# Optimization experiments

Measured on AMD Instinct MI355X. Metric: run time of the kernel, lower is better.

## Reference

```python
import jax, jax.numpy as jnp
import numpy as np

B, S, D = 2, 2048, 768          # batch, n_ctx, d_model
NQK, DQK = 12, 64               # n_qk_heads, d_qk_head
NOV, DOV = 768, 1               # n_ov_heads, d_ov_head
R = NOV // NQK                  # OV heads per QK head
VKV = 4                         # virtual_kv_num
BASE = 10000.0
SCALE = DQK ** 0.5              # cfg.attn_scale default


def _rotary_sin_cos():
    # TransformerLens-style (non-adjacent-pairs): freq repeated as (2 d)
    pos = jnp.arange(S, dtype=jnp.float32)
    freq = BASE ** (jnp.arange(0, DQK, 2, dtype=jnp.float32) / DQK)
    freq = jnp.concatenate([freq, freq])          # [DQK]
    angles = pos[:, None] / freq[None, :]         # [S, DQK]
    return jnp.sin(angles), jnp.cos(angles)


def _apply_rotary(x, sin, cos):
    # x: [b, pos, head, DQK]; rotary_dim == d_qk_head so full rotation
    half = DQK // 2
    rot = jnp.concatenate([-x[..., half:], x[..., :half]], axis=-1)
    return x * cos[None, :, None, :] + rot * sin[None, :, None, :]


def setup_inputs() -> dict:
    key = jax.random.key(0)
    ks = jax.random.split(key, 7)
    std_qk = (2.0 / (D * DQK)) ** 0.5   # kaiming fan_in (d_model*d_head)
    std_ov = (2.0 / (D * DOV)) ** 0.5
    std_o = (2.0 / (DOV * D)) ** 0.5
    sin, cos = _rotary_sin_cos()
    return {
        "resid": jax.random.normal(ks[0], (B, S, D), jnp.float32),
        "W_Q": jax.random.normal(ks[1], (NQK, D, DQK), jnp.float32) * std_qk,
        "W_K": jax.random.normal(ks[2], (NQK, D, DQK), jnp.float32) * std_qk,
        "W_V": jax.random.normal(ks[3], (NOV, D, DOV), jnp.float32) * std_ov,
        "W_O": jax.random.normal(ks[4], (NOV, DOV, D), jnp.float32) * std_o,
        "b_Q": jnp.zeros((NQK, DQK), jnp.float32),
        "b_K": jnp.zeros((NQK, DQK), jnp.float32),
        "b_V": jnp.zeros((NOV, DOV), jnp.float32),
        "virtual_k": jax.random.normal(ks[5], (VKV, NQK, DQK), jnp.float32) * (2.0 / (NQK * DQK)) ** 0.5,
        "virtual_v": jnp.zeros((VKV, NOV, DOV), jnp.float32),  # init zeros, requires_grad=False
        "rotary_sin": sin,
        "rotary_cos": cos,
    }


def reference(resid, W_Q, W_K, W_V, W_O, b_Q, b_K, b_V,
              virtual_k, virtual_v, rotary_sin, rotary_cos):
    # q/k/v projections: per-head low-rank maps + bias  -> [b, s, h, d]
    q = jnp.einsum('bsm,hmd->bshd', resid, W_Q) + b_Q
    k = jnp.einsum('bsm,hmd->bshd', resid, W_K) + b_K
    v = jnp.einsum('bsm,hmd->bshd', resid, W_V) + b_V
    # rotary on q and k
    q = _apply_rotary(q, rotary_sin, rotary_cos)
    k = _apply_rotary(k, rotary_sin, rotary_cos)
    # append virtual KV tokens at the end of the key axis
    k = jnp.concatenate([k, jnp.broadcast_to(virtual_k[None], (B, VKV, NQK, DQK))], axis=1)
    v = jnp.concatenate([v, jnp.broadcast_to(virtual_v[None], (B, VKV, NOV, DOV))], axis=1)
    # full attention scores [b, nqk, S, S+VKV]
    scores = jnp.einsum('bqhd,bkhd->bhqk', q, k) / SCALE
    # causal mask: tril(ones(S, S+VKV), diagonal=VKV) -> key j visible iff j <= i + VKV
    qi = jnp.arange(S)[:, None]
    kj = jnp.arange(S + VKV)[None, :]
    mask = kj <= qi + VKV
    scores = jnp.where(mask[None, None], scores, -jnp.inf)
    pattern = jax.nn.softmax(scores, axis=-1)
    pattern = jnp.where(jnp.isnan(pattern), 0.0, pattern)
    # group OV heads by QK head: v [b, k, NOV, DOV] -> [b, NQK, R, k, DOV]
    v_r = jnp.transpose(v, (0, 2, 1, 3)).reshape(B, NQK, R, S + VKV, DOV)
    z = jnp.einsum('bnqk,bnrkh->bnrqh', pattern, v_r)       # [b, NQK, R, S, DOV]
    z = z.reshape(B, NOV, S, DOV).transpose(0, 2, 1, 3)      # [b, S, NOV, DOV]
    out = jnp.einsum('bqhd,hdm->bqm', z, W_O)                # cal_out (no b_O)
    return out
```

## Files before the change

### kernel.cpp

```cpp
#include <hip/hip_runtime.h>

typedef __attribute__((ext_vector_type(8))) __bf16 bf16x8;
typedef __attribute__((ext_vector_type(4))) __bf16 bf16x4;
typedef __attribute__((ext_vector_type(4))) float  f32x4;

__device__ __forceinline__ void gld_lds16(const void* g, void* l) {
  __builtin_amdgcn_global_load_lds(
      (const __attribute__((address_space(1))) unsigned int*)g,
      (__attribute__((address_space(3))) unsigned int*)l, 16, 0, 0);
}

template<int N>
__device__ __forceinline__ void wait_vmcnt() {
  if constexpr (N == 0)      asm volatile("s_waitcnt vmcnt(0)" ::: "memory");
  else if constexpr (N == 4) asm volatile("s_waitcnt vmcnt(4)" ::: "memory");
  else if constexpr (N == 6) asm volatile("s_waitcnt vmcnt(6)" ::: "memory");
  else if constexpr (N == 8) asm volatile("s_waitcnt vmcnt(8)" ::: "memory");
}

#define QSCALE 0.18033688011112042f

__global__ __launch_bounds__(256) void prep_kernel(
    const float* __restrict__ resid, const float* __restrict__ WV,
    __bf16* __restrict__ Rb, __bf16* __restrict__ Wt1)
{
  int t = blockIdx.x * 256 + threadIdx.x;
  if (t < 786432) {
    f32x4 v = *(const f32x4*)(resid + (size_t)t * 4);
    bf16x4 o;
#pragma unroll
    for (int j = 0; j < 4; ++j) o[j] = (__bf16)v[j];
    *(bf16x4*)(Rb + (size_t)t * 4) = o;
    return;
  }
  t -= 786432;
  if (t < 73728) {
    const float* vp = WV + (size_t)t * 8;
    f32x4 v0 = *(const f32x4*)vp, v1 = *(const f32x4*)(vp + 4);
    bf16x8 o;
#pragma unroll
    for (int j = 0; j < 8; ++j) o[j] = (__bf16)((j < 4) ? v0[j & 3] : v1[j & 3]);
    *(bf16x8*)(Wt1 + (size_t)1536 * 768 + (size_t)t * 8) = o;
  }
}

__global__ __launch_bounds__(256) void wtrans_kernel(
    const float* __restrict__ WQ, const float* __restrict__ WK,
    const float* __restrict__ WO,
    __bf16* __restrict__ Wt1, __bf16* __restrict__ Wt2)
{
  __shared__ float tile[64][65];
  int g = blockIdx.x, tid = threadIdx.x;
  const float* src; __bf16* dst;
  int sld, dld, r0, c0, drow0, dcol0;
  if (g < 288) {
    const float* W = (g < 144) ? WQ : WK;
    int gg = g % 144;
    int h = gg / 12, kt = gg - h * 12;
    src = W + (size_t)h * 49152; sld = 64; r0 = kt * 64; c0 = 0;
    dst = Wt1; dld = 768;
    drow0 = ((g < 144) ? 0 : 768) + h * 64; dcol0 = kt * 64;
  } else {
    int gg = g - 288;
    int rt = gg / 12, ct = gg - rt * 12;
    src = WO; sld = 768; r0 = rt * 64; c0 = ct * 64;
    dst = Wt2; dld = 768; drow0 = ct * 64; dcol0 = rt * 64;
  }
#pragma unroll
  for (int c = 0; c < 4; ++c) {
    int li = c * 256 + tid;
    int r = li >> 4, cc = (li & 15) * 4;
    f32x4 v = *(const f32x4*)(src + (size_t)(r0 + r) * sld + c0 + cc);
#pragma unroll
    for (int j = 0; j < 4; ++j) tile[r][cc + j] = v[j];
  }
  __syncthreads();
#pragma unroll
  for (int c = 0; c < 2; ++c) {
    int li = c * 256 + tid;
    int cc = li >> 3, rr = (li & 7) * 8;
    bf16x8 o;
#pragma unroll
    for (int j = 0; j < 8; ++j) o[j] = (__bf16)tile[rr + j][cc];
    *(bf16x8*)(dst + (size_t)(drow0 + cc) * dld + dcol0 + rr) = o;
  }
}

template<int OUTF, int BN>
__global__ __launch_bounds__(256) void gemm_bt(
    const __bf16* __restrict__ A, const __bf16* __restrict__ Bt,
    void* __restrict__ C, int M, int N, int K, int ldc)
{
  constexpr int LDSB = BN * 128;
  constexpr int BUF  = 16384 + LDSB;
  constexpr int BSTG = BN / 32;
  constexpr int NLD  = 4 + BSTG;
  constexpr int IM   = (BN == 128) ? 4 : 2;
  __shared__ __align__(16) char smem[2 * BUF];
  const int tid = threadIdx.x;
  const int l = tid & 63, wv = tid >> 6;
  const int l15 = l & 15, lg = l >> 4;
  const int wmb = (BN == 128) ? (wv >> 1) * 64 : wv * 32;
  const int wnb = (BN == 128) ? (wv & 1) * 64 : 0;
  const int m0 = blockIdx.y * 128, n0 = blockIdx.x * BN;
  const int sw = (l15 & 7) << 4;

  auto stage = [&](int buf, int k0) {
    char* a_l = smem + buf * BUF;
    char* b_l = a_l + 16384;
#pragma unroll
    for (int c = 0; c < 4; ++c) {
      int i2 = c * 256 + tid;
      int row = i2 >> 3, slt = i2 & 7;
      gld_lds16(A + (size_t)(m0 + row) * K + k0 + ((slt ^ (row & 7)) * 8), a_l + i2 * 16);
    }
#pragma unroll
    for (int c = 0; c < BSTG; ++c) {
      int i2 = c * 256 + tid;
      int row = i2 >> 3, slt = i2 & 7;
      gld_lds16(Bt + (size_t)(n0 + row) * K + k0 + ((slt ^ (row & 7)) * 8), b_l + i2 * 16);
    }
  };

  f32x4 acc[IM][4] = {};
  stage(0, 0);
  int cur = 0;
  for (int k0 = 0; k0 < K; k0 += 64) {
    const bool has_next = (k0 + 64 < K);
    if (has_next) stage(cur ^ 1, k0 + 64);
    if (has_next) wait_vmcnt<NLD>(); else wait_vmcnt<0>();
    __builtin_amdgcn_s_barrier();
    __builtin_amdgcn_sched_barrier(0);
    char* a_lds = smem + cur * BUF;
    char* b_lds = a_lds + 16384;
#pragma unroll
    for (int kk = 0; kk < 2; ++kk) {
      bf16x8 af[IM], bfr[4];
#pragma unroll
      for (int i = 0; i < IM; ++i) {
        int mr = wmb + i * 16 + l15;
        af[i] = *(const bf16x8*)(a_lds + mr * 128 + ((lg * 16 + kk * 64) ^ sw));
      }
#pragma unroll
      for (int j = 0; j < 4; ++j) {
        int nr = wnb + j * 16 + l15;
        bfr[j] = *(const bf16x8*)(b_lds + nr * 128 + ((lg * 16 + kk * 64) ^ sw));
      }
#pragma unroll
      for (int i = 0; i < IM; ++i)
#pragma unroll
        for (int j = 0; j < 4; ++j)
          acc[i][j] = __builtin_amdgcn_mfma_f32_16x16x32_bf16(af[i], bfr[j], acc[i][j], 0, 0, 0);
    }
    __builtin_amdgcn_s_barrier();
    cur ^= 1;
  }
#pragma unroll
  for (int i = 0; i < IM; ++i)
#pragma unroll
    for (int j = 0; j < 4; ++j)
#pragma unroll
      for (int r = 0; r < 4; ++r) {
        int row = m0 + wmb + i * 16 + lg * 4 + r;
        int col = n0 + wnb + j * 16 + l15;
        if (OUTF) ((float*)C)[(size_t)row * ldc + col] = acc[i][j][r];
        else      ((__bf16*)C)[(size_t)row * ldc + col] = (__bf16)acc[i][j][r];
      }
}

__global__ __launch_bounds__(256) void qk_rotary(
    const __bf16* __restrict__ qkv, const float* __restrict__ bQ,
    const float* __restrict__ bK, const float* __restrict__ vk,
    const float* __restrict__ rsin, const float* __restrict__ rcos,
    __bf16* __restrict__ Qb, __bf16* __restrict__ Kb)
{
  int t = blockIdx.x * 256 + threadIdx.x;
  if (t < 196608) {
    int d0 = (t & 3) * 8;
    int x = t >> 2;
    int bh = x >> 11, s = x & 2047;
    int b = bh / 12, h = bh - b * 12;
    const __bf16* rowp = qkv + ((size_t)(b * 2048 + s)) * 2304 + h * 64;
    bf16x8 ql = *(const bf16x8*)(rowp + d0);
    bf16x8 qu = *(const bf16x8*)(rowp + d0 + 32);
    bf16x8 kl = *(const bf16x8*)(rowp + 768 + d0);
    bf16x8 ku = *(const bf16x8*)(rowp + 768 + d0 + 32);
    const float* bql = bQ + h * 64 + d0;
    const float* bkl = bK + h * 64 + d0;
    const float* snp = rsin + s * 64 + d0;
    const float* csp = rcos + s * 64 + d0;
    f32x4 bq0 = *(const f32x4*)(bql),      bq1 = *(const f32x4*)(bql + 4);
    f32x4 bq2 = *(const f32x4*)(bql + 32), bq3 = *(const f32x4*)(bql + 36);
    f32x4 bk0 = *(const f32x4*)(bkl),      bk1 = *(const f32x4*)(bkl + 4);
    f32x4 bk2 = *(const f32x4*)(bkl + 32), bk3 = *(const f32x4*)(bkl + 36);
    f32x4 sl0 = *(const f32x4*)(snp),      sl1 = *(const f32x4*)(snp + 4);
    f32x4 su0 = *(const f32x4*)(snp + 32), su1 = *(const f32x4*)(snp + 36);
    f32x4 cl0 = *(const f32x4*)(csp),      cl1 = *(const f32x4*)(csp + 4);
    f32x4 cu0 = *(const f32x4*)(csp + 32), cu1 = *(const f32x4*)(csp + 36);
    bf16x8 qlo, quo, klo, kuo;
#pragma unroll
    for (int j = 0; j < 8; ++j) {
      float snl = (j < 4) ? sl0[j & 3] : sl1[j & 3];
      float csl = (j < 4) ? cl0[j & 3] : cl1[j & 3];
      float snu = (j < 4) ? su0[j & 3] : su1[j & 3];
      float csu = (j < 4) ? cu0[j & 3] : cu1[j & 3];
      float q1 = (float)ql[j] + ((j < 4) ? bq0[j & 3] : bq1[j & 3]);
      float q2 = (float)qu[j] + ((j < 4) ? bq2[j & 3] : bq3[j & 3]);
      float k1 = (float)kl[j] + ((j < 4) ? bk0[j & 3] : bk1[j & 3]);
      float k2 = (float)ku[j] + ((j < 4) ? bk2[j & 3] : bk3[j & 3]);
      qlo[j] = (__bf16)((q1 * csl - q2 * snl) * QSCALE);
      quo[j] = (__bf16)((q2 * csu + q1 * snu) * QSCALE);
      klo[j] = (__bf16)(k1 * csl - k2 * snl);
      kuo[j] = (__bf16)(k2 * csu + k1 * snu);
    }
    __bf16* qb = Qb + ((size_t)bh * 2048 + s) * 64;
    __bf16* kb = Kb + ((size_t)bh * 2112 + s) * 64;
    *(bf16x8*)(qb + d0) = qlo;  *(bf16x8*)(qb + d0 + 32) = quo;
    *(bf16x8*)(kb + d0) = klo;  *(bf16x8*)(kb + d0 + 32) = kuo;
    return;
  }
  t -= 196608;
  if (t < 12288) {
    int d0 = (t & 7) * 8;
    int x = t >> 3;
    int bh = x >> 6, sp = x & 63;
    int h = bh % 12;
    bf16x8 o;
    if (sp < 4) {
      const float* vp = vk + ((size_t)sp * 12 + h) * 64 + d0;
      f32x4 v0 = *(const f32x4*)(vp), v1 = *(const f32x4*)(vp + 4);
#pragma unroll
      for (int j = 0; j < 8; ++j) o[j] = (__bf16)((j < 4) ? v0[j & 3] : v1[j & 3]);
    } else {
#pragma unroll
      for (int j = 0; j < 8; ++j) o[j] = (__bf16)0.0f;
    }
    *(bf16x8*)(Kb + ((size_t)bh * 2112 + 2048 + sp) * 64 + d0) = o;
  }
}

__global__ __launch_bounds__(256) void v_trans(
    const __bf16* __restrict__ qkv, const float* __restrict__ bV,
    const float* __restrict__ vv, __bf16* __restrict__ Vt)
{
  __shared__ float tile[64][65];
  int st = blockIdx.x, bh = blockIdx.y;
  int b = bh / 12, h = bh - b * 12;
  int tid = threadIdx.x;
#pragma unroll
  for (int c = 0; c < 2; ++c) {
    int chunk = c * 256 + tid;
    int srow = chunk >> 3, d0 = (chunk & 7) * 8;
    int s = st * 64 + srow;
    float vals[8];
    if (s < 2048) {
      bf16x8 v8 = *(const bf16x8*)(qkv + ((size_t)(b * 2048 + s)) * 2304 + 1536 + h * 64 + d0);
      const float* bvp = bV + h * 64 + d0;
      f32x4 b0 = *(const f32x4*)(bvp), b1 = *(const f32x4*)(bvp + 4);
#pragma unroll
      for (int j = 0; j < 8; ++j) vals[j] = (float)v8[j] + ((j < 4) ? b0[j & 3] : b1[j & 3]);
    } else if (s < 2052) {
      const float* vp = vv + (size_t)(s - 2048) * 768 + h * 64 + d0;
      f32x4 v0 = *(const f32x4*)(vp), v1 = *(const f32x4*)(vp + 4);
#pragma unroll
      for (int j = 0; j < 8; ++j) vals[j] = (j < 4) ? v0[j & 3] : v1[j & 3];
    } else {
#pragma unroll
      for (int j = 0; j < 8; ++j) vals[j] = 0.0f;
    }
#pragma unroll
    for (int j = 0; j < 8; ++j) tile[srow][d0 + j] = vals[j];
  }
  __syncthreads();
#pragma unroll
  for (int c = 0; c < 2; ++c) {
    int chunk = c * 256 + tid;
    int drow = chunk >> 3, s0 = (chunk & 7) * 8;
    bf16x8 o8;
#pragma unroll
    for (int j = 0; j < 8; ++j) o8[j] = (__bf16)tile[s0 + j][drow];
    *(bf16x8*)(Vt + ((size_t)bh * 64 + drow) * 2112 + st * 64 + s0) = o8;
  }
}

__global__ __launch_bounds__(256) void attn_kernel(
    const __bf16* __restrict__ Qb, const __bf16* __restrict__ Kb,
    const __bf16* __restrict__ Vt, __bf16* __restrict__ Opart,
    float* __restrict__ Lsum)
{
  __shared__ __align__(16) char smem[40960];
  char* p_lds = smem + 32768;
  const int tid = threadIdx.x;
  const int l = tid & 63, w = tid >> 6;
  const int l15 = l & 15, lg = l >> 4;
  const int idx = blockIdx.x;
  const int bh = idx % 24;
  int pidx = idx / 24;
  int qt = 31, rem = pidx;
  for (;;) { int c = (qt + 9) >> 3; if (rem < c) break; rem -= c; --qt; }
  const int ts = rem * 8;
  const int te = min(ts + 8, qt + 2);
  const int slot = bh * 84 + pidx;
  const int q16 = qt * 64 + w * 16;
  const int sw = (l15 & 7) << 4;
  const int qrow = w * 16 + l15;

  const __bf16* Kbase = Kb + (size_t)bh * 2112 * 64;
  const __bf16* Vbase = Vt + (size_t)bh * 64 * 2112;

  auto stage = [&](int buf, int kt0) {
    char* k_l = smem + buf * 16384;
    char* v_l = k_l + 8192;
#pragma unroll
    for (int c = 0; c < 2; ++c) {
      int i2 = c * 256 + tid;
      int row = i2 >> 3, slt = i2 & 7;
      gld_lds16(Kbase + (kt0 + row) * 64 + ((slt ^ (row & 7)) * 8), k_l + i2 * 16);
    }
#pragma unroll
    for (int c = 0; c < 2; ++c) {
      int i2 = c * 256 + tid;
      int row = i2 >> 3, slt = i2 & 7;
      gld_lds16(Vbase + row * 2112 + kt0 + ((slt ^ (row & 7)) * 8), v_l + i2 * 16);
    }
  };

  stage(0, ts * 64);

  const __bf16* qp = Qb + ((size_t)bh * 2048 + q16 + l15) * 64 + lg * 8;
  const bf16x8 qa0 = *(const bf16x8*)qp;
  const bf16x8 qa1 = *(const bf16x8*)(qp + 32);

  f32x4 o[4] = {};
  float lrun = 0.0f;

  int cur = 0;
  for (int kt = ts; kt < te; ++kt) {
    const int kt0 = kt * 64;
    const bool has_next = (kt + 1 < te);
    if (has_next) stage(cur ^ 1, kt0 + 64);
    if (has_next) wait_vmcnt<4>(); else wait_vmcnt<0>();
    __builtin_amdgcn_s_barrier();
    __builtin_amdgcn_sched_barrier(0);
    char* k_lds = smem + cur * 16384;
    char* v_lds = k_lds + 8192;

    if (kt0 <= q16 + 19) {
      f32x4 sfr[4];
#pragma unroll
      for (int kb = 0; kb < 4; ++kb) {
        int krow = kb * 16 + l15;
        f32x4 a = {};
        bf16x8 ka0 = *(const bf16x8*)(k_lds + krow * 128 + ((lg * 16) ^ sw));
        bf16x8 ka1 = *(const bf16x8*)(k_lds + krow * 128 + ((lg * 16 + 64) ^ sw));
        a = __builtin_amdgcn_mfma_f32_16x16x32_bf16(ka0, qa0, a, 0, 0, 0);
        a = __builtin_amdgcn_mfma_f32_16x16x32_bf16(ka1, qa1, a, 0, 0, 0);
        sfr[kb] = a;
      }
      if (kt >= qt) {
        int qlim = q16 + l15 + 4;
#pragma unroll
        for (int kb = 0; kb < 4; ++kb)
#pragma unroll
          for (int r = 0; r < 4; ++r) {
            int kg = kt0 + kb * 16 + lg * 4 + r;
            if (kg > qlim || kg >= 2052) sfr[kb][r] = -1e30f;
          }
      }
      float rsum = 0.0f;
#pragma unroll
      for (int kb = 0; kb < 4; ++kb) {
        bf16x4 pv;
#pragma unroll
        for (int r = 0; r < 4; ++r) {
          float p = exp2f(sfr[kb][r]);
          rsum += p;
          pv[r] = (__bf16)p;
        }
        *(bf16x4*)(p_lds + qrow * 128 + ((kb * 32 + lg * 8) ^ sw)) = pv;
      }
      rsum += __shfl_xor(rsum, 16);
      rsum += __shfl_xor(rsum, 32);
      lrun += rsum;
#pragma unroll
      for (int kblk = 0; kblk < 2; ++kblk) {
        bf16x8 pa = *(const bf16x8*)(p_lds + qrow * 128 + ((kblk * 64 + lg * 16) ^ sw));
#pragma unroll
        for (int dv = 0; dv < 4; ++dv) {
          int vrow = dv * 16 + l15;
          bf16x8 vb = *(const bf16x8*)(v_lds + vrow * 128 + ((kblk * 64 + lg * 16) ^ sw));
          o[dv] = __builtin_amdgcn_mfma_f32_16x16x32_bf16(pa, vb, o[dv], 0, 0, 0);
        }
      }
    }
    __builtin_amdgcn_s_barrier();
    cur ^= 1;
  }
  if (lg == 0) Lsum[slot * 64 + qrow] = lrun;
  __bf16* op = Opart + (size_t)slot * 4096;
#pragma unroll
  for (int dv = 0; dv < 4; ++dv)
#pragma unroll
    for (int r = 0; r < 4; ++r)
      op[(w * 16 + lg * 4 + r) * 64 + dv * 16 + l15] = (__bf16)o[dv][r];
}

__global__ __launch_bounds__(256) void attn_merge(
    const __bf16* __restrict__ Opart, const float* __restrict__ Lsum,
    __bf16* __restrict__ Z)
{
  const int idx = blockIdx.x;
  const int bh = idx % 24, qt = idx / 24;
  const int b = bh / 12, n = bh - b * 12;
  int pbase = 0;
  for (int q2 = 31; q2 > qt; --q2) pbase += (q2 + 9) >> 3;
  const int ns = (qt + 9) >> 3;
  const int t = threadIdx.x;
  const int q = t >> 2, c0 = (t & 3) * 16;

  float L = 0.0f;
  float acc[16] = {};
  for (int s = 0; s < ns; ++s) {
    int slot = bh * 84 + pbase + s;
    L += Lsum[slot * 64 + q];
    const __bf16* op = Opart + (size_t)slot * 4096 + q * 64 + c0;
    bf16x8 o0 = *(const bf16x8*)op, o1 = *(const bf16x8*)(op + 8);
#pragma unroll
    for (int j = 0; j < 8; ++j) {
      acc[j]     += (float)o0[j];
      acc[8 + j] += (float)o1[j];
    }
  }
  float inv = 1.0f / L;
  bf16x8 z0, z1;
#pragma unroll
  for (int j = 0; j < 8; ++j) {
    z0[j] = (__bf16)(acc[j] * inv);
    z1[j] = (__bf16)(acc[8 + j] * inv);
  }
  __bf16* zp = Z + ((size_t)(b * 2048 + qt * 64 + q)) * 768 + n * 64 + c0;
  *(bf16x8*)zp = z0;
  *(bf16x8*)(zp + 8) = z1;
}

extern "C" void kernel_launch(void* const* d_in, const int* in_sizes, int n_in,
                              void* d_out, int out_size, void* d_ws, size_t ws_size,
                              hipStream_t stream)
{
  const float* resid = (const float*)d_in[0];
  const float* WQ   = (const float*)d_in[1];
  const float* WK   = (const float*)d_in[2];
  const float* WV   = (const float*)d_in[3];
  const float* WO   = (const float*)d_in[4];
  const float* bQ   = (const float*)d_in[5];
  const float* bK   = (const float*)d_in[6];
  const float* bV   = (const float*)d_in[7];
  const float* vk   = (const float*)d_in[8];
  const float* vv   = (const float*)d_in[9];
  const float* rsin = (const float*)d_in[10];
  const float* rcos = (const float*)d_in[11];

  char* ws = (char*)d_ws;
  __bf16* Rb  = (__bf16*)(ws);
  __bf16* Wt1 = (__bf16*)(ws + 6291456);
  __bf16* Wt2 = (__bf16*)(ws + 9830400);
  __bf16* QKV = (__bf16*)(ws + 11010048);
  __bf16* Qb  = (__bf16*)(ws + 29884416);
  __bf16* Kb  = (__bf16*)(ws + 36175872);
  __bf16* Vt  = (__bf16*)(ws + 42663936);
  __bf16* Zb  = (__bf16*)(ws + 49152000);
  __bf16* Opart = (__bf16*)(ws + 11010048);
  float*  Lp    = (float*)(ws + 11010048 + 16515072);

  prep_kernel<<<3360, 256, 0, stream>>>(resid, WV, Rb, Wt1);
  wtrans_kernel<<<432, 256, 0, stream>>>(WQ, WK, WO, Wt1, Wt2);
  gemm_bt<0, 128><<<dim3(18, 32), 256, 0, stream>>>(Rb, Wt1, (void*)QKV, 4096, 2304, 768, 2304);
  qk_rotary<<<816, 256, 0, stream>>>(QKV, bQ, bK, vk, rsin, rcos, Qb, Kb);
  v_trans<<<dim3(33, 24), 256, 0, stream>>>(QKV, bV, vv, Vt);
  attn_kernel<<<2016, 256, 0, stream>>>(Qb, Kb, Vt, Opart, Lp);
  attn_merge<<<768, 256, 0, stream>>>(Opart, Lp, Zb);
  gemm_bt<1, 64><<<dim3(12, 32), 256, 0, stream>>>(Zb, Wt2, d_out, 4096, 768, 768, 768);
}
```

Baseline: 179.7 us.

## Fuse prep kernels, fuse rotary with V transpose, merge partials inside attention

Combines the resid/W_V conversion and weight transpose into one launch that also zeroes a counter array, and merges qk_rotary with v_trans into a single launch. The attention kernel writes Z directly when a query tile has only one split. Otherwise the last split block to finish, found with an atomic counter after a threadfence, does the cross-split merge, so the separate merge kernel is removed. This cuts launch count and inter-kernel gaps, at the cost of atomics, fences and a tail merge done by a single block.

```diff
diff --git a/kernel.cpp b/kernel.cpp
--- a/kernel.cpp
+++ b/kernel.cpp
@@ -20,37 +20,39 @@
 
 #define QSCALE 0.18033688011112042f
 
-__global__ __launch_bounds__(256) void prep_kernel(
+__global__ __launch_bounds__(256) void prep_all(
     const float* __restrict__ resid, const float* __restrict__ WV,
-    __bf16* __restrict__ Rb, __bf16* __restrict__ Wt1)
-{
-  int t = blockIdx.x * 256 + threadIdx.x;
-  if (t < 786432) {
-    f32x4 v = *(const f32x4*)(resid + (size_t)t * 4);
-    bf16x4 o;
-#pragma unroll
-    for (int j = 0; j < 4; ++j) o[j] = (__bf16)v[j];
-    *(bf16x4*)(Rb + (size_t)t * 4) = o;
-    return;
-  }
-  t -= 786432;
-  if (t < 73728) {
-    const float* vp = WV + (size_t)t * 8;
-    f32x4 v0 = *(const f32x4*)vp, v1 = *(const f32x4*)(vp + 4);
-    bf16x8 o;
-#pragma unroll
-    for (int j = 0; j < 8; ++j) o[j] = (__bf16)((j < 4) ? v0[j & 3] : v1[j & 3]);
-    *(bf16x8*)(Wt1 + (size_t)1536 * 768 + (size_t)t * 8) = o;
-  }
-}
-
-__global__ __launch_bounds__(256) void wtrans_kernel(
     const float* __restrict__ WQ, const float* __restrict__ WK,
     const float* __restrict__ WO,
-    __bf16* __restrict__ Wt1, __bf16* __restrict__ Wt2)
+    __bf16* __restrict__ Rb, __bf16* __restrict__ Wt1, __bf16* __restrict__ Wt2,
+    int* __restrict__ Cnt)
 {
   __shared__ float tile[64][65];
-  int g = blockIdx.x, tid = threadIdx.x;
+  const int bid = blockIdx.x, tid = threadIdx.x;
+  if (bid < 3360) {
+    int t = bid * 256 + tid;
+    if (t < 786432) {
+      f32x4 v = *(const f32x4*)(resid + (size_t)t * 4);
+      bf16x4 o;
+#pragma unroll
+      for (int j = 0; j < 4; ++j) o[j] = (__bf16)v[j];
+      *(bf16x4*)(Rb + (size_t)t * 4) = o;
+    } else {
+      t -= 786432;
+      const float* vp = WV + (size_t)t * 8;
+      f32x4 v0 = *(const f32x4*)vp, v1 = *(const f32x4*)(vp + 4);
+      bf16x8 o;
+#pragma unroll
+      for (int j = 0; j < 8; ++j) o[j] = (__bf16)((j < 4) ? v0[j & 3] : v1[j & 3]);
+      *(bf16x8*)(Wt1 + (size_t)1536 * 768 + (size_t)t * 8) = o;
+    }
+    return;
+  }
+  if (bid >= 3792) {
+    for (int i = tid; i < 768; i += 256) Cnt[i] = 0;
+    return;
+  }
+  int g = bid - 3360;
   const float* src; __bf16* dst;
   int sld, dld, r0, c0, drow0, dcol0;
   if (g < 288) {
@@ -168,85 +170,84 @@
       }
 }
 
-__global__ __launch_bounds__(256) void qk_rotary(
+__global__ __launch_bounds__(256) void qk_vt(
     const __bf16* __restrict__ qkv, const float* __restrict__ bQ,
-    const float* __restrict__ bK, const float* __restrict__ vk,
+    const float* __restrict__ bK, const float* __restrict__ bV,
+    const float* __restrict__ vk, const float* __restrict__ vv,
     const float* __restrict__ rsin, const float* __restrict__ rcos,
-    __bf16* __restrict__ Qb, __bf16* __restrict__ Kb)
-{
-  int t = blockIdx.x * 256 + threadIdx.x;
-  if (t < 196608) {
-    int d0 = (t & 3) * 8;
-    int x = t >> 2;
-    int bh = x >> 11, s = x & 2047;
-    int b = bh / 12, h = bh - b * 12;
-    const __bf16* rowp = qkv + ((size_t)(b * 2048 + s)) * 2304 + h * 64;
-    bf16x8 ql = *(const bf16x8*)(rowp + d0);
-    bf16x8 qu = *(const bf16x8*)(rowp + d0 + 32);
-    bf16x8 kl = *(const bf16x8*)(rowp + 768 + d0);
-    bf16x8 ku = *(const bf16x8*)(rowp + 768 + d0 + 32);
-    const float* bql = bQ + h * 64 + d0;
-    const float* bkl = bK + h * 64 + d0;
-    const float* snp = rsin + s * 64 + d0;
-    const float* csp = rcos + s * 64 + d0;
-    f32x4 bq0 = *(const f32x4*)(bql),      bq1 = *(const f32x4*)(bql + 4);
-    f32x4 bq2 = *(const f32x4*)(bql + 32), bq3 = *(const f32x4*)(bql + 36);
-    f32x4 bk0 = *(const f32x4*)(bkl),      bk1 = *(const f32x4*)(bkl + 4);
-    f32x4 bk2 = *(const f32x4*)(bkl + 32), bk3 = *(const f32x4*)(bkl + 36);
-    f32x4 sl0 = *(const f32x4*)(snp),      sl1 = *(const f32x4*)(snp + 4);
-    f32x4 su0 = *(const f32x4*)(snp + 32), su1 = *(const f32x4*)(snp + 36);
-    f32x4 cl0 = *(const f32x4*)(csp),      cl1 = *(const f32x4*)(csp + 4);
-    f32x4 cu0 = *(const f32x4*)(csp + 32), cu1 = *(const f32x4*)(csp + 36);
-    bf16x8 qlo, quo, klo, kuo;
-#pragma unroll
-    for (int j = 0; j < 8; ++j) {
-      float snl = (j < 4) ? sl0[j & 3] : sl1[j & 3];
-      float csl = (j < 4) ? cl0[j & 3] : cl1[j & 3];
-      float snu = (j < 4) ? su0[j & 3] : su1[j & 3];
-      float csu = (j < 4) ? cu0[j & 3] : cu1[j & 3];
-      float q1 = (float)ql[j] + ((j < 4) ? bq0[j & 3] : bq1[j & 3]);
-      float q2 = (float)qu[j] + ((j < 4) ? bq2[j & 3] : bq3[j & 3]);
-      float k1 = (float)kl[j] + ((j < 4) ? bk0[j & 3] : bk1[j & 3]);
-      float k2 = (float)ku[j] + ((j < 4) ? bk2[j & 3] : bk3[j & 3]);
-      qlo[j] = (__bf16)((q1 * csl - q2 * snl) * QSCALE);
-      quo[j] = (__bf16)((q2 * csu + q1 * snu) * QSCALE);
-      klo[j] = (__bf16)(k1 * csl - k2 * snl);
-      kuo[j] = (__bf16)(k2 * csu + k1 * snu);
-    }
-    __bf16* qb = Qb + ((size_t)bh * 2048 + s) * 64;
-    __bf16* kb = Kb + ((size_t)bh * 2112 + s) * 64;
-    *(bf16x8*)(qb + d0) = qlo;  *(bf16x8*)(qb + d0 + 32) = quo;
-    *(bf16x8*)(kb + d0) = klo;  *(bf16x8*)(kb + d0 + 32) = kuo;
-    return;
-  }
-  t -= 196608;
-  if (t < 12288) {
-    int d0 = (t & 7) * 8;
-    int x = t >> 3;
-    int bh = x >> 6, sp = x & 63;
-    int h = bh % 12;
-    bf16x8 o;
-    if (sp < 4) {
-      const float* vp = vk + ((size_t)sp * 12 + h) * 64 + d0;
-      f32x4 v0 = *(const f32x4*)(vp), v1 = *(const f32x4*)(vp + 4);
-#pragma unroll
-      for (int j = 0; j < 8; ++j) o[j] = (__bf16)((j < 4) ? v0[j & 3] : v1[j & 3]);
-    } else {
-#pragma unroll
-      for (int j = 0; j < 8; ++j) o[j] = (__bf16)0.0f;
-    }
-    *(bf16x8*)(Kb + ((size_t)bh * 2112 + 2048 + sp) * 64 + d0) = o;
-  }
-}
-
-__global__ __launch_bounds__(256) void v_trans(
-    const __bf16* __restrict__ qkv, const float* __restrict__ bV,
-    const float* __restrict__ vv, __bf16* __restrict__ Vt)
+    __bf16* __restrict__ Qb, __bf16* __restrict__ Kb, __bf16* __restrict__ Vt)
 {
   __shared__ float tile[64][65];
-  int st = blockIdx.x, bh = blockIdx.y;
+  const int bid = blockIdx.x, tid = threadIdx.x;
+  if (bid < 816) {
+    int t = bid * 256 + tid;
+    if (t < 196608) {
+      int d0 = (t & 3) * 8;
+      int x = t >> 2;
+      int bh = x >> 11, s = x & 2047;
+      int b = bh / 12, h = bh - b * 12;
+      const __bf16* rowp = qkv + ((size_t)(b * 2048 + s)) * 2304 + h * 64;
+      bf16x8 ql = *(const bf16x8*)(rowp + d0);
+      bf16x8 qu = *(const bf16x8*)(rowp + d0 + 32);
+      bf16x8 kl = *(const bf16x8*)(rowp + 768 + d0);
+      bf16x8 ku = *(const bf16x8*)(rowp + 768 + d0 + 32);
+      const float* bql = bQ + h * 64 + d0;
+      const float* bkl = bK + h * 64 + d0;
+      const float* snp = rsin + s * 64 + d0;
+      const float* csp = rcos + s * 64 + d0;
+      f32x4 bq0 = *(const f32x4*)(bql),      bq1 = *(const f32x4*)(bql + 4);
+      f32x4 bq2 = *(const f32x4*)(bql + 32), bq3 = *(const f32x4*)(bql + 36);
+      f32x4 bk0 = *(const f32x4*)(bkl),      bk1 = *(const f32x4*)(bkl + 4);
+      f32x4 bk2 = *(const f32x4*)(bkl + 32), bk3 = *(const f32x4*)(bkl + 36);
+      f32x4 sl0 = *(const f32x4*)(snp),      sl1 = *(const f32x4*)(snp + 4);
+      f32x4 su0 = *(const f32x4*)(snp + 32), su1 = *(const f32x4*)(snp + 36);
+      f32x4 cl0 = *(const f32x4*)(csp),      cl1 = *(const f32x4*)(csp + 4);
+      f32x4 cu0 = *(const f32x4*)(csp + 32), cu1 = *(const f32x4*)(csp + 36);
+      bf16x8 qlo, quo, klo, kuo;
+#pragma unroll
+      for (int j = 0; j < 8; ++j) {
+        float snl = (j < 4) ? sl0[j & 3] : sl1[j & 3];
+        float csl = (j < 4) ? cl0[j & 3] : cl1[j & 3];
+        float snu = (j < 4) ? su0[j & 3] : su1[j & 3];
+        float csu = (j < 4) ? cu0[j & 3] : cu1[j & 3];
+        float q1 = (float)ql[j] + ((j < 4) ? bq0[j & 3] : bq1[j & 3]);
+        float q2 = (float)qu[j] + ((j < 4) ? bq2[j & 3] : bq3[j & 3]);
+        float k1 = (float)kl[j] + ((j < 4) ? bk0[j & 3] : bk1[j & 3]);
+        float k2 = (float)ku[j] + ((j < 4) ? bk2[j & 3] : bk3[j & 3]);
+        qlo[j] = (__bf16)((q1 * csl - q2 * snl) * QSCALE);
+        quo[j] = (__bf16)((q2 * csu + q1 * snu) * QSCALE);
+        klo[j] = (__bf16)(k1 * csl - k2 * snl);
+        kuo[j] = (__bf16)(k2 * csu + k1 * snu);
+      }
+      __bf16* qb = Qb + ((size_t)bh * 2048 + s) * 64;
+      __bf16* kb = Kb + ((size_t)bh * 2112 + s) * 64;
+      *(bf16x8*)(qb + d0) = qlo;  *(bf16x8*)(qb + d0 + 32) = quo;
+      *(bf16x8*)(kb + d0) = klo;  *(bf16x8*)(kb + d0 + 32) = kuo;
+    } else {
+      t -= 196608;
+      if (t < 12288) {
+        int d0 = (t & 7) * 8;
+        int x = t >> 3;
+        int bh = x >> 6, sp = x & 63;
+        int h = bh % 12;
+        bf16x8 o;
+        if (sp < 4) {
+          const float* vp = vk + ((size_t)sp * 12 + h) * 64 + d0;
+          f32x4 v0 = *(const f32x4*)(vp), v1 = *(const f32x4*)(vp + 4);
+#pragma unroll
+          for (int j = 0; j < 8; ++j) o[j] = (__bf16)((j < 4) ? v0[j & 3] : v1[j & 3]);
+        } else {
+#pragma unroll
+          for (int j = 0; j < 8; ++j) o[j] = (__bf16)0.0f;
+        }
+        *(bf16x8*)(Kb + ((size_t)bh * 2112 + 2048 + sp) * 64 + d0) = o;
+      }
+    }
+    return;
+  }
+  int g = bid - 816;
+  int st = g % 33, bh = g / 33;
   int b = bh / 12, h = bh - b * 12;
-  int tid = threadIdx.x;
 #pragma unroll
   for (int c = 0; c < 2; ++c) {
     int chunk = c * 256 + tid;
@@ -286,9 +287,10 @@
 __global__ __launch_bounds__(256) void attn_kernel(
     const __bf16* __restrict__ Qb, const __bf16* __restrict__ Kb,
     const __bf16* __restrict__ Vt, __bf16* __restrict__ Opart,
-    float* __restrict__ Lsum)
+    float* __restrict__ Lsum, int* __restrict__ Cnt, __bf16* __restrict__ Z)
 {
   __shared__ __align__(16) char smem[40960];
+  __shared__ int lastflag;
   char* p_lds = smem + 32768;
   const int tid = threadIdx.x;
   const int l = tid & 63, w = tid >> 6;
@@ -300,7 +302,9 @@
   for (;;) { int c = (qt + 9) >> 3; if (rem < c) break; rem -= c; --qt; }
   const int ts = rem * 8;
   const int te = min(ts + 8, qt + 2);
+  const int ns = (qt + 9) >> 3;
   const int slot = bh * 84 + pidx;
+  const int b = bh / 12, n = bh - b * 12;
   const int q16 = qt * 64 + w * 16;
   const int sw = (l15 & 7) << 4;
   const int qrow = w * 16 + l15;
@@ -396,6 +400,21 @@
     __builtin_amdgcn_s_barrier();
     cur ^= 1;
   }
+
+  if (ns == 1) {
+    float linv = 1.0f / lrun;
+    f32x4 lv;
+#pragma unroll
+    for (int r = 0; r < 4; ++r) lv[r] = __shfl(linv, lg * 4 + r);
+    __bf16* zbase = Z + ((size_t)(b * 2048 + q16)) * 768 + n * 64;
+#pragma unroll
+    for (int dv = 0; dv < 4; ++dv)
+#pragma unroll
+      for (int r = 0; r < 4; ++r)
+        zbase[(lg * 4 + r) * 768 + dv * 16 + l15] = (__bf16)(o[dv][r] * lv[r]);
+    return;
+  }
+
   if (lg == 0) Lsum[slot * 64 + qrow] = lrun;
   __bf16* op = Opart + (size_t)slot * 4096;
 #pragma unroll
@@ -403,28 +422,27 @@
 #pragma unroll
     for (int r = 0; r < 4; ++r)
       op[(w * 16 + lg * 4 + r) * 64 + dv * 16 + l15] = (__bf16)o[dv][r];
-}
-
-__global__ __launch_bounds__(256) void attn_merge(
-    const __bf16* __restrict__ Opart, const float* __restrict__ Lsum,
-    __bf16* __restrict__ Z)
-{
-  const int idx = blockIdx.x;
-  const int bh = idx % 24, qt = idx / 24;
-  const int b = bh / 12, n = bh - b * 12;
-  int pbase = 0;
-  for (int q2 = 31; q2 > qt; --q2) pbase += (q2 + 9) >> 3;
-  const int ns = (qt + 9) >> 3;
-  const int t = threadIdx.x;
-  const int q = t >> 2, c0 = (t & 3) * 16;
-
+
+  __threadfence();
+  __syncthreads();
+  if (tid == 0) {
+    int prev = atomicAdd(&Cnt[bh * 32 + qt], 1);
+    lastflag = (prev == ns - 1);
+  }
+  __syncthreads();
+  if (!lastflag) return;
+  __threadfence();
+
+  int pb = 0;
+  for (int q2 = 31; q2 > qt; --q2) pb += (q2 + 9) >> 3;
+  const int q = tid >> 2, c0 = (tid & 3) * 16;
   float L = 0.0f;
   float acc[16] = {};
   for (int s = 0; s < ns; ++s) {
-    int slot = bh * 84 + pbase + s;
-    L += Lsum[slot * 64 + q];
-    const __bf16* op = Opart + (size_t)slot * 4096 + q * 64 + c0;
-    bf16x8 o0 = *(const bf16x8*)op, o1 = *(const bf16x8*)(op + 8);
+    int sl2 = bh * 84 + pb + s;
+    L += Lsum[sl2 * 64 + q];
+    const __bf16* op2 = Opart + (size_t)sl2 * 4096 + q * 64 + c0;
+    bf16x8 o0 = *(const bf16x8*)op2, o1 = *(const bf16x8*)(op2 + 8);
 #pragma unroll
     for (int j = 0; j < 8; ++j) {
       acc[j]     += (float)o0[j];
@@ -471,13 +489,11 @@
   __bf16* Zb  = (__bf16*)(ws + 49152000);
   __bf16* Opart = (__bf16*)(ws + 11010048);
   float*  Lp    = (float*)(ws + 11010048 + 16515072);
-
-  prep_kernel<<<3360, 256, 0, stream>>>(resid, WV, Rb, Wt1);
-  wtrans_kernel<<<432, 256, 0, stream>>>(WQ, WK, WO, Wt1, Wt2);
+  int*    Cnt   = (int*)(ws + 56623104);
+
+  prep_all<<<3793, 256, 0, stream>>>(resid, WV, WQ, WK, WO, Rb, Wt1, Wt2, Cnt);
   gemm_bt<0, 128><<<dim3(18, 32), 256, 0, stream>>>(Rb, Wt1, (void*)QKV, 4096, 2304, 768, 2304);
-  qk_rotary<<<816, 256, 0, stream>>>(QKV, bQ, bK, vk, rsin, rcos, Qb, Kb);
-  v_trans<<<dim3(33, 24), 256, 0, stream>>>(QKV, bV, vv, Vt);
-  attn_kernel<<<2016, 256, 0, stream>>>(Qb, Kb, Vt, Opart, Lp);
-  attn_merge<<<768, 256, 0, stream>>>(Opart, Lp, Zb);
+  qk_vt<<<1608, 256, 0, stream>>>(QKV, bQ, bK, bV, vk, vv, rsin, rcos, Qb, Kb, Vt);
+  attn_kernel<<<2016, 256, 0, stream>>>(Qb, Kb, Vt, Opart, Lp, Cnt, Zb);
   gemm_bt<1, 64><<<dim3(12, 32), 256, 0, stream>>>(Zb, Wt2, d_out, 4096, 768, 768, 768);
 }
```

Result: slower. 479.4 us (+166.7%).
